# Kernel optimization log

Measured on AMD Instinct MI355X. Metric: run time of the kernel, lower is better.

## Reference

```python
import jax, jax.numpy as jnp
import numpy as np

B, H, V, L = 1024, 2048, 8192, 8


def setup_inputs() -> dict:
    key = jax.random.key(0)
    k1, k2, k3, k4 = jax.random.split(key, 4)
    state = jax.random.normal(k1, (B, H), dtype=jnp.float32)
    token = jax.random.randint(k2, (B,), 0, V, dtype=jnp.int64)
    ih = jax.random.normal(k3, (L, V, H), dtype=jnp.float32) * 0.02
    hh = jax.random.normal(k4, (L, H, H), dtype=jnp.float32) * 0.02
    return {"state": state, "token": token, "ih": ih, "hh": hh}


def reference(state, token, ih, hh):
    # Per layer: state = tanh(state + (state @ hh[i]) * ih[i][token])
    # ih[i][token]: gather -> [B, H]; state @ hh[i]: [B,H]@[H,H] -> [B,H]
    def step(s, layer_params):
        hh_i, ih_i = layer_params
        gate = ih_i[token]                      # [B, H] embedding gather
        s = jnp.tanh(s + (s @ hh_i) * gate)     # fused mul-add-tanh
        return s, None

    state, _ = jax.lax.scan(step, state, (hh, ih))
    return state
```

## Files before the change

kernel.cpp:

```cpp
#include <hip/hip_runtime.h>
#include <hip/hip_bf16.h>

#define B_DIM 1024
#define H_DIM 2048
#define V_DIM 8192
#define L_DIM 8

typedef __attribute__((ext_vector_type(8))) __bf16 bf16x8;
typedef __attribute__((ext_vector_type(4))) __bf16 bf16x4;
typedef __attribute__((ext_vector_type(4))) float f32x4;
typedef unsigned short u16;

__device__ __forceinline__ void async_copy16(const void* g, void* l) {
  __builtin_amdgcn_global_load_lds(
      (const unsigned int __attribute__((address_space(1)))*)g,
      (unsigned int __attribute__((address_space(3)))*)l,
      16, 0, 0);
}

__global__ __launch_bounds__(256) void conv_state_kernel(
    const float4* __restrict__ in, bf16x4* __restrict__ out) {
  int i = blockIdx.x * 256 + threadIdx.x;
  float4 v = in[i];
  bf16x4 o;
  o.x = (__bf16)v.x; o.y = (__bf16)v.y; o.z = (__bf16)v.z; o.w = (__bf16)v.w;
  out[i] = o;
}

__global__ __launch_bounds__(256) void hh_transpose_kernel(
    const float* __restrict__ hh_l, __bf16* __restrict__ hhT) {
  int t = blockIdx.x;
  int k0 = (t >> 5) << 6;
  int n0 = (t & 31) << 6;
  __shared__ __bf16 tile[64][67];
  int tid = threadIdx.x;
  {
    int r = tid >> 2;
    int c = (tid & 3) << 4;
    const float4* src = (const float4*)(hh_l + (size_t)(k0 + r) * H_DIM + n0 + c);
#pragma unroll
    for (int q = 0; q < 4; q++) {
      float4 v = src[q];
      tile[r][c + q * 4 + 0] = (__bf16)v.x;
      tile[r][c + q * 4 + 1] = (__bf16)v.y;
      tile[r][c + q * 4 + 2] = (__bf16)v.z;
      tile[r][c + q * 4 + 3] = (__bf16)v.w;
    }
  }
  __syncthreads();
  {
    int n = tid >> 2;
    int kq = (tid & 3) << 4;
    alignas(16) u16 tmp[16];
#pragma unroll
    for (int j = 0; j < 16; j++) {
      __bf16 b = tile[kq + j][n];
      tmp[j] = *(const u16*)&b;
    }
    uint4* dst = (uint4*)(hhT + (size_t)(n0 + n) * H_DIM + k0 + kq);
    dst[0] = *(uint4*)(tmp);
    dst[1] = *(uint4*)(tmp + 8);
  }
}

__global__ __launch_bounds__(256) void rnn_layer_kernel(
    const __bf16* __restrict__ A, const __bf16* __restrict__ Bt,
    const float* __restrict__ S, const float* __restrict__ ih_l,
    const int* __restrict__ token,
    float* __restrict__ OutF, __bf16* __restrict__ OutB) {
  constexpr int K = H_DIM;
  __shared__ __align__(16) __bf16 As[64 * 64];
  __shared__ __align__(16) __bf16 Bs[64 * 64];

  int bid = blockIdx.x;
  int x = bid & 7;
  int rest = bid >> 3;
  int mi = rest & 15;
  int ni = (rest >> 4) * 8 + x;
  int bm0 = mi * 64;
  int bn0 = ni * 64;

  int tid = threadIdx.x;
  int w = tid >> 6;
  int lane = tid & 63;
  int rsub = lane >> 3;
  int csw = (lane & 7) ^ rsub;

  const __bf16* pA0 = A + (size_t)(bm0 + (w * 2 + 0) * 8 + rsub) * K + csw * 8;
  const __bf16* pA1 = A + (size_t)(bm0 + (w * 2 + 1) * 8 + rsub) * K + csw * 8;
  const __bf16* pB0 = Bt + (size_t)(bn0 + (w * 2 + 0) * 8 + rsub) * K + csw * 8;
  const __bf16* pB1 = Bt + (size_t)(bn0 + (w * 2 + 1) * 8 + rsub) * K + csw * 8;
  __bf16* lA0 = As + (w * 2 + 0) * 512;
  __bf16* lA1 = As + (w * 2 + 1) * 512;
  __bf16* lB0 = Bs + (w * 2 + 0) * 512;
  __bf16* lB1 = Bs + (w * 2 + 1) * 512;

  int wm = (w >> 1) * 32;
  int wn = (w & 1) * 32;
  int col = lane & 15;
  int quad = lane >> 4;
  int c7 = lane & 7;

  f32x4 acc[2][2] = {};

  for (int kt = 0; kt < K; kt += 64) {
    __syncthreads();
    async_copy16(pA0 + kt, lA0);
    async_copy16(pA1 + kt, lA1);
    async_copy16(pB0 + kt, lB0);
    async_copy16(pB1 + kt, lB1);
    __syncthreads();
#pragma unroll
    for (int ks = 0; ks < 2; ks++) {
      int cc = ks * 4 + quad;
      bf16x8 a0 = *(const bf16x8*)(As + (wm + 0 + col) * 64 + ((cc ^ c7) * 8));
      bf16x8 a1 = *(const bf16x8*)(As + (wm + 16 + col) * 64 + ((cc ^ c7) * 8));
      bf16x8 b0 = *(const bf16x8*)(Bs + (wn + 0 + col) * 64 + ((cc ^ c7) * 8));
      bf16x8 b1 = *(const bf16x8*)(Bs + (wn + 16 + col) * 64 + ((cc ^ c7) * 8));
      acc[0][0] = __builtin_amdgcn_mfma_f32_16x16x32_bf16(a0, b0, acc[0][0], 0, 0, 0);
      acc[0][1] = __builtin_amdgcn_mfma_f32_16x16x32_bf16(a0, b1, acc[0][1], 0, 0, 0);
      acc[1][0] = __builtin_amdgcn_mfma_f32_16x16x32_bf16(a1, b0, acc[1][0], 0, 0, 0);
      acc[1][1] = __builtin_amdgcn_mfma_f32_16x16x32_bf16(a1, b1, acc[1][1], 0, 0, 0);
    }
  }

#pragma unroll
  for (int mt = 0; mt < 2; mt++) {
#pragma unroll
    for (int reg = 0; reg < 4; reg++) {
      int b = bm0 + wm + mt * 16 + quad * 4 + reg;
      int tok = token[b];
      const float* ihrow = ih_l + (size_t)tok * H_DIM;
      size_t rowoff = (size_t)b * H_DIM;
#pragma unroll
      for (int nt = 0; nt < 2; nt++) {
        int h = bn0 + wn + nt * 16 + col;
        float g = ihrow[h];
        float sv = S[rowoff + h];
        float v = tanhf(fmaf(acc[mt][nt][reg], g, sv));
        OutF[rowoff + h] = v;
        OutB[rowoff + h] = (__bf16)v;
      }
    }
  }
}

extern "C" void kernel_launch(void* const* d_in, const int* in_sizes, int n_in,
                              void* d_out, int out_size, void* d_ws, size_t ws_size,
                              hipStream_t stream) {
  const float* state = (const float*)d_in[0];
  const int* token = (const int*)d_in[1];
  const float* ih = (const float*)d_in[2];
  const float* hh = (const float*)d_in[3];

  char* ws = (char*)d_ws;
  __bf16* hhT = (__bf16*)ws;
  float* F0 = (float*)(ws + 8388608);
  float* F1 = (float*)(ws + 16777216);
  __bf16* Sb0 = (__bf16*)(ws + 25165824);
  __bf16* Sb1 = (__bf16*)(ws + 29360128);

  conv_state_kernel<<<2048, 256, 0, stream>>>((const float4*)state, (bf16x4*)Sb0);

  const float* Sprev = state;
  for (int l = 0; l < L_DIM; l++) {
    const float* hh_l = hh + ((size_t)l << 22);
    const float* ih_l = ih + ((size_t)l << 24);
    hh_transpose_kernel<<<1024, 256, 0, stream>>>(hh_l, hhT);

    const __bf16* Acur = (l & 1) ? Sb1 : Sb0;
    __bf16* outB = (l & 1) ? Sb0 : Sb1;
    float* outF = (l == L_DIM - 1) ? (float*)d_out : ((l & 1) ? F1 : F0);
    rnn_layer_kernel<<<512, 256, 0, stream>>>(Acur, hhT, Sprev, ih_l, token, outF, outB);
    Sprev = outF;
  }
}
```

Before: 941.8 us.

## Double-buffer LDS tiles in RNN GEMM and batch all weight transposes

The GEMM main loop now uses two LDS buffers and issues async global-to-LDS loads for the next k-tile while computing the current one. Manual vmcnt waits and raw s_barrier replace the two __syncthreads per iteration. All eight hh transposes now run in one launch into a larger workspace, which removes seven small launches and their serialization between layer GEMMs. The cost is double the LDS per block and a workspace of about 90 MB, and correctness depends on the hand-placed waitcnt/barrier ordering.

Result: no change. 924.3 us (-1.9%).

```diff
diff --git a/kernel.cpp b/kernel.cpp
--- a/kernel.cpp
+++ b/kernel.cpp
@@ -10,6 +10,10 @@
 typedef __attribute__((ext_vector_type(4))) __bf16 bf16x4;
 typedef __attribute__((ext_vector_type(4))) float f32x4;
 typedef unsigned short u16;
+
+#define ASM_BARRIER() asm volatile("s_barrier" ::: "memory")
+#define WAIT_VM4() asm volatile("s_waitcnt vmcnt(4)" ::: "memory")
+#define WAIT_VM0() asm volatile("s_waitcnt vmcnt(0)" ::: "memory")
 
 __device__ __forceinline__ void async_copy16(const void* g, void* l) {
   __builtin_amdgcn_global_load_lds(
@@ -18,7 +22,7 @@
       16, 0, 0);
 }
 
-__global__ __launch_bounds__(256) void conv_state_kernel(
+__global__ __launch_bounds__(256) void rnn_conv_state(
     const float4* __restrict__ in, bf16x4* __restrict__ out) {
   int i = blockIdx.x * 256 + threadIdx.x;
   float4 v = in[i];
@@ -27,13 +31,17 @@
   out[i] = o;
 }
 
-__global__ __launch_bounds__(256) void hh_transpose_kernel(
-    const float* __restrict__ hh_l, __bf16* __restrict__ hhT) {
-  int t = blockIdx.x;
+__global__ __launch_bounds__(256) void rnn_hh_transpose_all(
+    const float* __restrict__ hh, __bf16* __restrict__ hhT) {
+  int bid = blockIdx.x;
+  int l = bid >> 10;
+  int t = bid & 1023;
   int k0 = (t >> 5) << 6;
   int n0 = (t & 31) << 6;
   __shared__ __bf16 tile[64][67];
   int tid = threadIdx.x;
+  const float* hh_l = hh + ((size_t)l << 22);
+  __bf16* hhT_l = hhT + ((size_t)l << 22);
   {
     int r = tid >> 2;
     int c = (tid & 3) << 4;
@@ -57,20 +65,21 @@
       __bf16 b = tile[kq + j][n];
       tmp[j] = *(const u16*)&b;
     }
-    uint4* dst = (uint4*)(hhT + (size_t)(n0 + n) * H_DIM + k0 + kq);
+    uint4* dst = (uint4*)(hhT_l + (size_t)(n0 + n) * H_DIM + k0 + kq);
     dst[0] = *(uint4*)(tmp);
     dst[1] = *(uint4*)(tmp + 8);
   }
 }
 
-__global__ __launch_bounds__(256) void rnn_layer_kernel(
+__global__ __launch_bounds__(256) void rnn_layer_pipe(
     const __bf16* __restrict__ A, const __bf16* __restrict__ Bt,
     const float* __restrict__ S, const float* __restrict__ ih_l,
     const int* __restrict__ token,
     float* __restrict__ OutF, __bf16* __restrict__ OutB) {
   constexpr int K = H_DIM;
-  __shared__ __align__(16) __bf16 As[64 * 64];
-  __shared__ __align__(16) __bf16 Bs[64 * 64];
+  constexpr int NT = K / 64;
+  __shared__ __align__(16) __bf16 As[2][64 * 64];
+  __shared__ __align__(16) __bf16 Bs[2][64 * 64];
 
   int bid = blockIdx.x;
   int x = bid & 7;
@@ -90,10 +99,8 @@
   const __bf16* pA1 = A + (size_t)(bm0 + (w * 2 + 1) * 8 + rsub) * K + csw * 8;
   const __bf16* pB0 = Bt + (size_t)(bn0 + (w * 2 + 0) * 8 + rsub) * K + csw * 8;
   const __bf16* pB1 = Bt + (size_t)(bn0 + (w * 2 + 1) * 8 + rsub) * K + csw * 8;
-  __bf16* lA0 = As + (w * 2 + 0) * 512;
-  __bf16* lA1 = As + (w * 2 + 1) * 512;
-  __bf16* lB0 = Bs + (w * 2 + 0) * 512;
-  __bf16* lB1 = Bs + (w * 2 + 1) * 512;
+  int slot0 = (w * 2 + 0) * 512;
+  int slot1 = (w * 2 + 1) * 512;
 
   int wm = (w >> 1) * 32;
   int wn = (w & 1) * 32;
@@ -103,25 +110,44 @@
 
   f32x4 acc[2][2] = {};
 
-  for (int kt = 0; kt < K; kt += 64) {
-    __syncthreads();
-    async_copy16(pA0 + kt, lA0);
-    async_copy16(pA1 + kt, lA1);
-    async_copy16(pB0 + kt, lB0);
-    async_copy16(pB1 + kt, lB1);
-    __syncthreads();
+  auto issue = [&](int buf, int kt) {
+    int ko = kt * 64;
+    async_copy16(pA0 + ko, &As[buf][slot0]);
+    async_copy16(pA1 + ko, &As[buf][slot1]);
+    async_copy16(pB0 + ko, &Bs[buf][slot0]);
+    async_copy16(pB1 + ko, &Bs[buf][slot1]);
+  };
+  auto compute = [&](int buf) {
 #pragma unroll
     for (int ks = 0; ks < 2; ks++) {
       int cc = ks * 4 + quad;
-      bf16x8 a0 = *(const bf16x8*)(As + (wm + 0 + col) * 64 + ((cc ^ c7) * 8));
-      bf16x8 a1 = *(const bf16x8*)(As + (wm + 16 + col) * 64 + ((cc ^ c7) * 8));
-      bf16x8 b0 = *(const bf16x8*)(Bs + (wn + 0 + col) * 64 + ((cc ^ c7) * 8));
-      bf16x8 b1 = *(const bf16x8*)(Bs + (wn + 16 + col) * 64 + ((cc ^ c7) * 8));
+      bf16x8 a0 = *(const bf16x8*)(&As[buf][(wm + 0 + col) * 64 + ((cc ^ c7) * 8)]);
+      bf16x8 a1 = *(const bf16x8*)(&As[buf][(wm + 16 + col) * 64 + ((cc ^ c7) * 8)]);
+      bf16x8 b0 = *(const bf16x8*)(&Bs[buf][(wn + 0 + col) * 64 + ((cc ^ c7) * 8)]);
+      bf16x8 b1 = *(const bf16x8*)(&Bs[buf][(wn + 16 + col) * 64 + ((cc ^ c7) * 8)]);
       acc[0][0] = __builtin_amdgcn_mfma_f32_16x16x32_bf16(a0, b0, acc[0][0], 0, 0, 0);
       acc[0][1] = __builtin_amdgcn_mfma_f32_16x16x32_bf16(a0, b1, acc[0][1], 0, 0, 0);
       acc[1][0] = __builtin_amdgcn_mfma_f32_16x16x32_bf16(a1, b0, acc[1][0], 0, 0, 0);
       acc[1][1] = __builtin_amdgcn_mfma_f32_16x16x32_bf16(a1, b1, acc[1][1], 0, 0, 0);
     }
+  };
+
+  issue(0, 0);
+  for (int kt = 0; kt < NT; kt += 2) {
+    issue(1, kt + 1);
+    WAIT_VM4();
+    ASM_BARRIER();
+    compute(0);
+    ASM_BARRIER();
+    if (kt + 2 < NT) {
+      issue(0, kt + 2);
+      WAIT_VM4();
+    } else {
+      WAIT_VM0();
+    }
+    ASM_BARRIER();
+    compute(1);
+    ASM_BARRIER();
   }
 
 #pragma unroll
@@ -155,23 +181,22 @@
 
   char* ws = (char*)d_ws;
   __bf16* hhT = (__bf16*)ws;
-  float* F0 = (float*)(ws + 8388608);
-  float* F1 = (float*)(ws + 16777216);
-  __bf16* Sb0 = (__bf16*)(ws + 25165824);
-  __bf16* Sb1 = (__bf16*)(ws + 29360128);
-
-  conv_state_kernel<<<2048, 256, 0, stream>>>((const float4*)state, (bf16x4*)Sb0);
+  float* F0 = (float*)(ws + 67108864);
+  float* F1 = (float*)(ws + 75497472);
+  __bf16* Sb0 = (__bf16*)(ws + 83886080);
+  __bf16* Sb1 = (__bf16*)(ws + 88080384);
+
+  rnn_hh_transpose_all<<<8192, 256, 0, stream>>>(hh, hhT);
+  rnn_conv_state<<<2048, 256, 0, stream>>>((const float4*)state, (bf16x4*)Sb0);
 
   const float* Sprev = state;
   for (int l = 0; l < L_DIM; l++) {
-    const float* hh_l = hh + ((size_t)l << 22);
+    const __bf16* hhT_l = hhT + ((size_t)l << 22);
     const float* ih_l = ih + ((size_t)l << 24);
-    hh_transpose_kernel<<<1024, 256, 0, stream>>>(hh_l, hhT);
-
     const __bf16* Acur = (l & 1) ? Sb1 : Sb0;
     __bf16* outB = (l & 1) ? Sb0 : Sb1;
     float* outF = (l == L_DIM - 1) ? (float*)d_out : ((l & 1) ? F1 : F0);
-    rnn_layer_kernel<<<512, 256, 0, stream>>>(Acur, hhT, Sprev, ih_l, token, outF, outB);
+    rnn_layer_pipe<<<512, 256, 0, stream>>>(Acur, hhT_l, Sprev, ih_l, token, outF, outB);
     Sprev = outF;
   }
 }
```
